# Optimization experiments

Measured on AMD Instinct MI355X. Metric: run time of the kernel, lower is better.

Reference implementation:

```python
import jax, jax.numpy as jnp
import numpy as np

N, E, F_IN, F_OUT = 20000, 8192, 128, 128


def setup_inputs() -> dict:
    key = jax.random.key(0)
    k1, k2, k3, k4, k5 = jax.random.split(key, 5)
    x = jax.random.normal(k1, (N, F_IN), dtype=jnp.float32)
    H = jax.random.uniform(k2, (N, E), dtype=jnp.float32)
    W = jax.random.uniform(k3, (E,), dtype=jnp.float32)  # diagonal of hyperedge weight matrix
    lin_w = jax.random.normal(k4, (F_OUT, F_IN), dtype=jnp.float32) * (1.0 / np.sqrt(F_IN))
    lin_b = jax.random.normal(k5, (F_OUT,), dtype=jnp.float32) * 0.01
    return {"x": x, "H": H, "W": W, "lin_w": lin_w, "lin_b": lin_b}


def reference(x, H, W, lin_w, lin_b):
    # Degrees
    Dv = jnp.clip(jnp.sum(H, axis=1), 1.0, None)          # [N] node degrees
    De = jnp.clip(jnp.sum(H, axis=0), 1.0, None)          # [E] hyperedge degrees
    dv_inv_sqrt = Dv ** -0.5                               # diag(Dv^-1/2)
    de_inv = 1.0 / De                                      # diag(De^-1)
    # Linear projection of node features
    xw = x @ lin_w.T + lin_b                               # [N, F_OUT]
    # L @ xw computed right-to-left: Dv^-1/2 H W De^-1 H^T Dv^-1/2 xw
    t = H.T @ (dv_inv_sqrt[:, None] * xw)                  # [E, F_OUT]
    t = (W * de_inv)[:, None] * t                          # diagonal W and De^-1 scaling
    out = dv_inv_sqrt[:, None] * (H @ t)                   # [N, F_OUT]
    return jax.nn.gelu(out, approximate=False)             # torch F.gelu default = exact erf
```

## Files before the change

### kernel.cpp

```cpp
#include <hip/hip_runtime.h>
#include <math.h>

static constexpr int N = 20000;
static constexpr int E = 8192;
static constexpr int F = 128;
static constexpr int NP = 20480;
static constexpr int NP2 = 20096;
static constexpr int PREP_BLOCKS = 1024;
static constexpr int PREP_REAL = 1000;
static constexpr int XW_BLOCKS = NP / 8;
static constexpr int SE_BLOCKS = 128;
static constexpr int KS_B = 8;
static constexpr int KS_C = 4;

typedef short bf16x8 __attribute__((ext_vector_type(8)));
typedef float f32x4 __attribute__((ext_vector_type(4)));

__device__ __forceinline__ float gelu_erf(float x) {
    return 0.5f * x * (1.0f + erff(x * 0.70710678118654752440f));
}
__device__ __forceinline__ ushort f2bf(float f) {
    unsigned u = __float_as_uint(f);
    return (ushort)((u + 0x7FFFu + ((u >> 16) & 1u)) >> 16);
}
__device__ __forceinline__ void gload16(const void* g, void* lds) {
    __builtin_amdgcn_global_load_lds(
        (const __attribute__((address_space(1))) unsigned int*)g,
        (__attribute__((address_space(3))) unsigned int*)lds, 16, 0, 0);
}

__global__ __launch_bounds__(256) void k_prep_xw(const float* __restrict__ H,
                                                 float* __restrict__ DeP,
                                                 ushort* __restrict__ Hbs,
                                                 const float* __restrict__ x,
                                                 const float* __restrict__ lin_w,
                                                 const float* __restrict__ lin_b,
                                                 ushort* __restrict__ yT) {
    __shared__ __align__(16) char smem[4096];
    const int tid = threadIdx.x;

    if (blockIdx.x < PREP_BLOCKS) {
        const int lane = tid & 63, wid = tid >> 6;
        const int r0 = blockIdx.x * 20;
        if (r0 >= N) {
            uint4 z = make_uint4(0, 0, 0, 0);
            for (int r = 0; r < 20; ++r) {
                ushort* orow = Hbs + (size_t)(r0 + r) * E;
#pragma unroll
                for (int j = 0; j < 4; ++j) *(uint4*)(orow + (j * 256 + tid) * 8) = z;
            }
            return;
        }
        float (*rp)[4] = (float(*)[4])smem;
        float4 ca[4][2];
#pragma unroll
        for (int j = 0; j < 4; ++j) {
            ca[j][0] = make_float4(0.f, 0.f, 0.f, 0.f);
            ca[j][1] = make_float4(0.f, 0.f, 0.f, 0.f);
        }
        for (int r = 0; r < 20; ++r) {
            const float* row = H + (size_t)(r0 + r) * E;
            float4 va[4], vb[4];
            float rs = 0.f;
#pragma unroll
            for (int j = 0; j < 4; ++j) {
                const float* base = row + (j * 256 + tid) * 8;
                va[j] = *(const float4*)(base);
                vb[j] = *(const float4*)(base + 4);
                ca[j][0].x += va[j].x; ca[j][0].y += va[j].y; ca[j][0].z += va[j].z; ca[j][0].w += va[j].w;
                ca[j][1].x += vb[j].x; ca[j][1].y += vb[j].y; ca[j][1].z += vb[j].z; ca[j][1].w += vb[j].w;
                rs += (va[j].x + va[j].y) + (va[j].z + va[j].w);
                rs += (vb[j].x + vb[j].y) + (vb[j].z + vb[j].w);
            }
#pragma unroll
            for (int off = 32; off > 0; off >>= 1) rs += __shfl_xor(rs, off, 64);
            if (lane == 0) rp[r][wid] = rs;
            __syncthreads();
            float scale = rsqrtf(fmaxf(rp[r][0] + rp[r][1] + rp[r][2] + rp[r][3], 1.f));
            ushort* orow = Hbs + (size_t)(r0 + r) * E;
#pragma unroll
            for (int j = 0; j < 4; ++j) {
                uint4 o;
                o.x = (unsigned)f2bf(va[j].x * scale) | ((unsigned)f2bf(va[j].y * scale) << 16);
                o.y = (unsigned)f2bf(va[j].z * scale) | ((unsigned)f2bf(va[j].w * scale) << 16);
                o.z = (unsigned)f2bf(vb[j].x * scale) | ((unsigned)f2bf(vb[j].y * scale) << 16);
                o.w = (unsigned)f2bf(vb[j].z * scale) | ((unsigned)f2bf(vb[j].w * scale) << 16);
                *(uint4*)(orow + (j * 256 + tid) * 8) = o;
            }
        }
        float* dp = DeP + (size_t)blockIdx.x * E;
#pragma unroll
        for (int j = 0; j < 4; ++j) {
            *(float4*)(dp + (j * 256 + tid) * 8) = ca[j][0];
            *(float4*)(dp + (j * 256 + tid) * 8 + 4) = ca[j][1];
        }
    } else {
        const int bxx = blockIdx.x - PREP_BLOCKS;
        const int r0 = bxx * 8;
        if (r0 >= N) {
            if (tid < 128) {
                uint4 z = make_uint4(0, 0, 0, 0);
                *(uint4*)(yT + (size_t)tid * NP + r0) = z;
            }
            return;
        }
        float* xs = (float*)smem;
#pragma unroll
        for (int c = 0; c < 4; ++c) {
            int lin = c * 256 + tid;
            xs[lin] = x[(size_t)r0 * F + lin];
        }
        __syncthreads();
        const int f = tid & 127, half = tid >> 7;
        float b = lin_b[f];
        float a0 = b, a1 = b, a2 = b, a3 = b;
        const float* xr = xs + (half * 4) * F;
        const float* lwr = lin_w + (size_t)f * F;
#pragma unroll 4
        for (int k = 0; k < F; k += 4) {
            float4 lw = *(const float4*)(lwr + k);
            a0 += xr[0 * F + k] * lw.x; a0 += xr[0 * F + k + 1] * lw.y;
            a0 += xr[0 * F + k + 2] * lw.z; a0 += xr[0 * F + k + 3] * lw.w;
            a1 += xr[1 * F + k] * lw.x; a1 += xr[1 * F + k + 1] * lw.y;
            a1 += xr[1 * F + k + 2] * lw.z; a1 += xr[1 * F + k + 3] * lw.w;
            a2 += xr[2 * F + k] * lw.x; a2 += xr[2 * F + k + 1] * lw.y;
            a2 += xr[2 * F + k + 2] * lw.z; a2 += xr[2 * F + k + 3] * lw.w;
            a3 += xr[3 * F + k] * lw.x; a3 += xr[3 * F + k + 1] * lw.y;
            a3 += xr[3 * F + k + 2] * lw.z; a3 += xr[3 * F + k + 3] * lw.w;
        }
        __syncthreads();
        ushort* tile = (ushort*)smem;
        tile[(half * 4 + 0) * F + f] = f2bf(a0);
        tile[(half * 4 + 1) * F + f] = f2bf(a1);
        tile[(half * 4 + 2) * F + f] = f2bf(a2);
        tile[(half * 4 + 3) * F + f] = f2bf(a3);
        __syncthreads();
        if (tid < 128) {
            unsigned u[4];
#pragma unroll
            for (int qq = 0; qq < 4; ++qq) {
                ushort lo = tile[(qq * 2 + 0) * F + tid];
                ushort hi = tile[(qq * 2 + 1) * F + tid];
                u[qq] = (unsigned)lo | ((unsigned)hi << 16);
            }
            uint4 o = make_uint4(u[0], u[1], u[2], u[3]);
            *(uint4*)(yT + (size_t)tid * NP + r0) = o;
        }
    }
}

__global__ void k_tst(const float* __restrict__ tB, const float* __restrict__ se,
                      ushort* __restrict__ tsT) {
    __shared__ __align__(16) char tl[8192];
    int tid = threadIdx.x;
    int r0 = (blockIdx.x >> 1) * 64;
    int c0 = (blockIdx.x & 1) * 64;
#pragma unroll
    for (int c = 0; c < 4; ++c) {
        int lin = c * 256 + tid;
        int row = lin >> 4, ch = lin & 15;
        size_t base = (size_t)(r0 + row) * F + c0 + ch * 4;
        float4 v = make_float4(0.f, 0.f, 0.f, 0.f);
#pragma unroll
        for (int ks = 0; ks < KS_B; ++ks) {
            float4 p = *(const float4*)(tB + (size_t)ks * E * F + base);
            v.x += p.x; v.y += p.y; v.z += p.z; v.w += p.w;
        }
        float s = se[r0 + row];
        ushort4 b;
        b.x = f2bf(v.x * s); b.y = f2bf(v.y * s); b.z = f2bf(v.z * s); b.w = f2bf(v.w * s);
        int key = ((row ^ (row >> 3)) & 7) << 4;
        *(ushort4*)(tl + row * 128 + ((ch * 8) ^ key)) = b;
    }
    __syncthreads();
#pragma unroll
    for (int c = 0; c < 2; ++c) {
        int lin = c * 256 + tid;
        int fl = lin >> 3, vch = lin & 7;
        unsigned u[4];
#pragma unroll
        for (int qq = 0; qq < 4; ++qq) {
            int r1 = vch * 8 + qq * 2, r2 = r1 + 1;
            ushort a = *(const ushort*)(tl + r1 * 128 + ((fl * 2) ^ (((r1 ^ (r1 >> 3)) & 7) << 4)));
            ushort b = *(const ushort*)(tl + r2 * 128 + ((fl * 2) ^ (((r2 ^ (r2 >> 3)) & 7) << 4)));
            u[qq] = (unsigned)a | ((unsigned)b << 16);
        }
        uint4 o = make_uint4(u[0], u[1], u[2], u[3]);
        *(uint4*)(tsT + (size_t)(c0 + fl) * E + r0 + vch * 8) = o;
    }
}

__global__ __launch_bounds__(256) void k_gemmB(const ushort* __restrict__ Hbs,
                                               const ushort* __restrict__ yT,
                                               float* __restrict__ tB,
                                               const float* __restrict__ DeP,
                                               const float* __restrict__ W,
                                               float* __restrict__ se) {
    __shared__ __align__(16) char lA[2][16384];
    __shared__ __align__(16) char lB[2][16384];
    const int tid = threadIdx.x;

    if (blockIdx.x < SE_BLOCKS) {
        float (*red)[64] = (float(*)[64])lA;
        const int c = blockIdx.x * 64 + (tid & 63);
        const int pg = tid >> 6;
        float s0 = 0.f, s1 = 0.f, s2 = 0.f, s3 = 0.f;
        int p = pg;
        for (; p + 12 < PREP_REAL; p += 16) {
            s0 += DeP[(size_t)(p +  0) * E + c];
            s1 += DeP[(size_t)(p +  4) * E + c];
            s2 += DeP[(size_t)(p +  8) * E + c];
            s3 += DeP[(size_t)(p + 12) * E + c];
        }
        for (; p < PREP_REAL; p += 4) s0 += DeP[(size_t)p * E + c];
        red[pg][tid & 63] = (s0 + s1) + (s2 + s3);
        __syncthreads();
        if (tid < 64) {
            float d = red[0][tid] + red[1][tid] + red[2][tid] + red[3][tid];
            int e = blockIdx.x * 64 + tid;
            se[e] = W[e] / fmaxf(d, 1.f);
        }
        return;
    }

    const int bx2 = blockIdx.x - SE_BLOCKS;
    const int sw = (bx2 & 7) * 64 + (bx2 >> 3);
    const int m0 = (sw & 63) * 128;
    const int ks = sw >> 6;
    const int k0 = ks * 2560;
    const int lane = tid & 63, w = tid >> 6;
    const int wm = (w & 1) * 64, wn = (w >> 1) * 64;
    const int lrow = lane & 15, g16 = (lane >> 4) * 16;
    const int NSTEP = 40;

    const int vq = tid >> 4;
    const int e8 = (tid & 15) * 8;
    const ushort* pa = Hbs + (size_t)(k0 + vq * 4) * E + m0 + e8;
    const int abase = e8 * 128 + ((vq * 8) ^ ((tid & 7) << 4));

    const int row8 = lane >> 3, ch8 = lane & 7;
    const ushort* gB = yT + (size_t)(w * 32 + row8) * NP + k0 + ((ch8 ^ row8) * 8);
    const int ldstB = w * 32 * 128;

    int aoff[4][2], boff[4][2];
#pragma unroll
    for (int f = 0; f < 4; ++f)
#pragma unroll
        for (int kk = 0; kk < 2; ++kk) {
            int ma = wm + f * 16 + lrow;
            aoff[f][kk] = ma * 128 + (((kk * 64) + g16) ^ (((ma >> 3) & 7) << 4));
            int nb = wn + f * 16 + lrow;
            boff[f][kk] = nb * 128 + (((kk * 64) + g16) ^ ((nb & 7) << 4));
        }

    f32x4 zero4 = {0.f, 0.f, 0.f, 0.f};
    f32x4 acc[4][4];
#pragma unroll
    for (int i = 0; i < 4; ++i)
#pragma unroll
        for (int j = 0; j < 4; ++j) acc[i][j] = zero4;

    uint4 ra[4];
#pragma unroll
    for (int r = 0; r < 4; ++r) ra[r] = *(const uint4*)(pa + (size_t)r * E);
    {
        const ushort* u0 = (const ushort*)&ra[0];
        const ushort* u1 = (const ushort*)&ra[1];
        const ushort* u2 = (const ushort*)&ra[2];
        const ushort* u3 = (const ushort*)&ra[3];
#pragma unroll
        for (int i = 0; i < 8; ++i) {
            uint2 wv;
            wv.x = (unsigned)u0[i] | ((unsigned)u1[i] << 16);
            wv.y = (unsigned)u2[i] | ((unsigned)u3[i] << 16);
            *(uint2*)(lA[0] + abase + i * 128) = wv;
        }
#pragma unroll
        for (int i = 0; i < 4; ++i)
            gload16(gB + (size_t)i * 8 * NP, lB[0] + ldstB + i * 1024);
    }
    pa += (size_t)64 * E;
#pragma unroll
    for (int r = 0; r < 4; ++r) ra[r] = *(const uint4*)(pa + (size_t)r * E);
    __syncthreads();

    for (int kt = 0; kt < NSTEP; ++kt) {
        const int cur = kt & 1;
        if (kt + 1 < NSTEP) {
            const ushort* u0 = (const ushort*)&ra[0];
            const ushort* u1 = (const ushort*)&ra[1];
            const ushort* u2 = (const ushort*)&ra[2];
            const ushort* u3 = (const ushort*)&ra[3];
#pragma unroll
            for (int i = 0; i < 8; ++i) {
                uint2 wv;
                wv.x = (unsigned)u0[i] | ((unsigned)u1[i] << 16);
                wv.y = (unsigned)u2[i] | ((unsigned)u3[i] << 16);
                *(uint2*)(lA[cur ^ 1] + abase + i * 128) = wv;
            }
            const int koff = (kt + 1) * 64;
#pragma unroll
            for (int i = 0; i < 4; ++i)
                gload16(gB + (size_t)i * 8 * NP + koff, lB[cur ^ 1] + ldstB + i * 1024);
        }
        if (kt + 2 < NSTEP) {
            pa += (size_t)64 * E;
#pragma unroll
            for (int r = 0; r < 4; ++r) ra[r] = *(const uint4*)(pa + (size_t)r * E);
        }
#pragma unroll
        for (int kk = 0; kk < 2; ++kk) {
            bf16x8 av[4], bv[4];
#pragma unroll
            for (int f = 0; f < 4; ++f) av[f] = *(const bf16x8*)(lA[cur] + aoff[f][kk]);
#pragma unroll
            for (int f = 0; f < 4; ++f) bv[f] = *(const bf16x8*)(lB[cur] + boff[f][kk]);
#pragma unroll
            for (int i = 0; i < 4; ++i)
#pragma unroll
                for (int j = 0; j < 4; ++j)
                    acc[i][j] = __builtin_amdgcn_mfma_f32_16x16x32_bf16(av[i], bv[j], acc[i][j], 0, 0, 0);
        }
        if (kt + 1 < NSTEP) __syncthreads();
    }
    float* plane = tB + (size_t)ks * E * F;
    const int orow = (lane >> 4) * 4, ocol = lane & 15;
#pragma unroll
    for (int i = 0; i < 4; ++i)
#pragma unroll
        for (int j = 0; j < 4; ++j) {
            int gm = m0 + wm + i * 16 + orow;
            int gn = wn + j * 16 + ocol;
#pragma unroll
            for (int q = 0; q < 4; ++q)
                plane[(size_t)(gm + q) * F + gn] = acc[i][j][q];
        }
}

__global__ __launch_bounds__(256) void k_gemmC(const ushort* __restrict__ Hbs,
                                               const ushort* __restrict__ tsT,
                                               float* __restrict__ C2P) {
    __shared__ __align__(16) char lA[2][16384];
    __shared__ __align__(16) char lB[2][16384];
    const int tid = threadIdx.x;
    const int qq_ = 78, rr_ = 4;
    const int xcd = blockIdx.x & 7, idx = blockIdx.x >> 3;
    const int sw = (xcd < rr_ ? xcd * (qq_ + 1) : rr_ * (qq_ + 1) + (xcd - rr_) * qq_) + idx;
    const int m0 = (sw % 157) * 128;
    const int ks = sw / 157;
    const int k0 = ks * 2048;
    const int lane = tid & 63, w = tid >> 6;
    const int wm = (w & 1) * 64, wn = (w >> 1) * 64;
    const int lrow = lane & 15, g16 = (lane >> 4) * 16;
    const int NSTEP = 32;

    const int row8 = lane >> 3, ch8 = lane & 7;
    const ushort* gA = Hbs + (size_t)(m0 + w * 32 + row8) * E + k0 + ((ch8 ^ row8) * 8);
    const ushort* gB = tsT + (size_t)(w * 32 + row8) * E + k0 + ((ch8 ^ row8) * 8);
    const int ldst = w * 32 * 128;

    int aoff[4][2], boff[4][2];
#pragma unroll
    for (int f = 0; f < 4; ++f)
#pragma unroll
        for (int kk = 0; kk < 2; ++kk) {
            int ma = wm + f * 16 + lrow;
            aoff[f][kk] = ma * 128 + (((kk * 64) + g16) ^ ((ma & 7) << 4));
            int nb = wn + f * 16 + lrow;
            boff[f][kk] = nb * 128 + (((kk * 64) + g16) ^ ((nb & 7) << 4));
        }

    f32x4 zero4 = {0.f, 0.f, 0.f, 0.f};
    f32x4 acc[4][4];
#pragma unroll
    for (int i = 0; i < 4; ++i)
#pragma unroll
        for (int j = 0; j < 4; ++j) acc[i][j] = zero4;

#pragma unroll
    for (int i = 0; i < 4; ++i) {
        gload16(gA + (size_t)i * 8 * E, lA[0] + ldst + i * 1024);
        gload16(gB + (size_t)i * 8 * E, lB[0] + ldst + i * 1024);
    }
    __syncthreads();

    for (int kt = 0; kt < NSTEP; ++kt) {
        const int cur = kt & 1;
        if (kt + 1 < NSTEP) {
            const int koff = (kt + 1) * 64;
#pragma unroll
            for (int i = 0; i < 4; ++i) {
                gload16(gA + (size_t)i * 8 * E + koff, lA[cur ^ 1] + ldst + i * 1024);
                gload16(gB + (size_t)i * 8 * E + koff, lB[cur ^ 1] + ldst + i * 1024);
            }
        }
#pragma unroll
        for (int kk = 0; kk < 2; ++kk) {
            bf16x8 av[4], bv[4];
#pragma unroll
            for (int f = 0; f < 4; ++f) av[f] = *(const bf16x8*)(lA[cur] + aoff[f][kk]);
#pragma unroll
            for (int f = 0; f < 4; ++f) bv[f] = *(const bf16x8*)(lB[cur] + boff[f][kk]);
#pragma unroll
            for (int i = 0; i < 4; ++i)
#pragma unroll
                for (int j = 0; j < 4; ++j)
                    acc[i][j] = __builtin_amdgcn_mfma_f32_16x16x32_bf16(av[i], bv[j], acc[i][j], 0, 0, 0);
        }
        if (kt + 1 < NSTEP) __syncthreads();
    }
    float* plane = C2P + (size_t)ks * NP2 * F;
    const int orow = (lane >> 4) * 4, ocol = lane & 15;
#pragma unroll
    for (int i = 0; i < 4; ++i)
#pragma unroll
        for (int j = 0; j < 4; ++j) {
            int gm = m0 + wm + i * 16 + orow;
            int gn = wn + j * 16 + ocol;
#pragma unroll
            for (int q = 0; q < 4; ++q)
                plane[(size_t)(gm + q) * F + gn] = acc[i][j][q];
        }
}

__global__ void k_fin_out(const float* __restrict__ C2P, float* __restrict__ out) {
    int i4 = blockIdx.x * 256 + threadIdx.x;
    if (i4 < N * F / 4) {
        float4 v = make_float4(0.f, 0.f, 0.f, 0.f);
#pragma unroll
        for (int ks = 0; ks < KS_C; ++ks) {
            float4 p = reinterpret_cast<const float4*>(C2P + (size_t)ks * NP2 * F)[i4];
            v.x += p.x; v.y += p.y; v.z += p.z; v.w += p.w;
        }
        float4 o;
        o.x = gelu_erf(v.x);
        o.y = gelu_erf(v.y);
        o.z = gelu_erf(v.z);
        o.w = gelu_erf(v.w);
        reinterpret_cast<float4*>(out)[i4] = o;
    }
}

extern "C" void kernel_launch(void* const* d_in, const int* in_sizes, int n_in,
                              void* d_out, int out_size, void* d_ws, size_t ws_size,
                              hipStream_t stream) {
    const float* x     = (const float*)d_in[0];
    const float* H     = (const float*)d_in[1];
    const float* W     = (const float*)d_in[2];
    const float* lin_w = (const float*)d_in[3];
    const float* lin_b = (const float*)d_in[4];
    float* out = (float*)d_out;

    char* ws = (char*)d_ws;
    ushort* Hbs = (ushort*)ws;
    ushort* yT  = (ushort*)(ws + 335544320);
    float*  tB  = (float*) (ws + 340787200);
    ushort* tsT = (ushort*)(ws + 374341632);
    float*  C2P = (float*) (ws + 376438784);
    float*  DeP = (float*) (ws + 417595392);
    float*  se  = (float*) (ws + 451149824);

    k_prep_xw<<<PREP_BLOCKS + XW_BLOCKS, 256, 0, stream>>>(H, DeP, Hbs, x, lin_w, lin_b, yT);
    k_gemmB<<<SE_BLOCKS + 64 * KS_B, 256, 0, stream>>>(Hbs, yT, tB, DeP, W, se);
    k_tst<<<(E / 64) * 2, 256, 0, stream>>>(tB, se, tsT);
    k_gemmC<<<157 * KS_C, 256, 0, stream>>>(Hbs, tsT, C2P);
    k_fin_out<<<(N * F / 4 + 255) / 256, 256, 0, stream>>>(C2P, out);
}
```

Baseline: 461.7 us.

## Store unscaled bf16 H and compute hyperedge degrees with MFMA in gemmB

H is now stored as raw bf16 without the per-row Dv^-1/2 scale. The Dv^-1/2 factor moves onto the projected features (new k_yscale kernel) and onto the final output before GELU. The per-block column partial sums and the separate SE reduction blocks are removed. Hyperedge degrees are instead accumulated inside gemmB with an extra MFMA against a ones vector, and the partials are summed in k_tst. This removes the 1000-row DeP partial buffer traffic and the in-prep syncs, in exchange for one extra small kernel, more MFMA work, and De computed from bf16-rounded H values.

```diff
diff --git a/kernel.cpp b/kernel.cpp
--- a/kernel.cpp
+++ b/kernel.cpp
@@ -6,10 +6,8 @@
 static constexpr int F = 128;
 static constexpr int NP = 20480;
 static constexpr int NP2 = 20096;
-static constexpr int PREP_BLOCKS = 1024;
-static constexpr int PREP_REAL = 1000;
+static constexpr int PREP_BLOCKS = 2048;
 static constexpr int XW_BLOCKS = NP / 8;
-static constexpr int SE_BLOCKS = 128;
 static constexpr int KS_B = 8;
 static constexpr int KS_C = 4;
 
@@ -19,9 +17,9 @@
 __device__ __forceinline__ float gelu_erf(float x) {
     return 0.5f * x * (1.0f + erff(x * 0.70710678118654752440f));
 }
-__device__ __forceinline__ ushort f2bf(float f) {
+__device__ __forceinline__ unsigned f2bf(float f) {
     unsigned u = __float_as_uint(f);
-    return (ushort)((u + 0x7FFFu + ((u >> 16) & 1u)) >> 16);
+    return (u + 0x7FFFu + ((u >> 16) & 1u)) >> 16;
 }
 __device__ __forceinline__ void gload16(const void* g, void* lds) {
     __builtin_amdgcn_global_load_lds(
@@ -30,7 +28,7 @@
 }
 
 __global__ __launch_bounds__(256) void k_prep_xw(const float* __restrict__ H,
-                                                 float* __restrict__ DeP,
+                                                 float* __restrict__ Dv,
                                                  ushort* __restrict__ Hbs,
                                                  const float* __restrict__ x,
                                                  const float* __restrict__ lin_w,
@@ -41,10 +39,10 @@
 
     if (blockIdx.x < PREP_BLOCKS) {
         const int lane = tid & 63, wid = tid >> 6;
-        const int r0 = blockIdx.x * 20;
+        const int r0 = blockIdx.x * 10;
         if (r0 >= N) {
             uint4 z = make_uint4(0, 0, 0, 0);
-            for (int r = 0; r < 20; ++r) {
+            for (int r = 0; r < 10; ++r) {
                 ushort* orow = Hbs + (size_t)(r0 + r) * E;
 #pragma unroll
                 for (int j = 0; j < 4; ++j) *(uint4*)(orow + (j * 256 + tid) * 8) = z;
@@ -52,48 +50,30 @@
             return;
         }
         float (*rp)[4] = (float(*)[4])smem;
-        float4 ca[4][2];
-#pragma unroll
-        for (int j = 0; j < 4; ++j) {
-            ca[j][0] = make_float4(0.f, 0.f, 0.f, 0.f);
-            ca[j][1] = make_float4(0.f, 0.f, 0.f, 0.f);
-        }
-        for (int r = 0; r < 20; ++r) {
+        for (int r = 0; r < 10; ++r) {
             const float* row = H + (size_t)(r0 + r) * E;
-            float4 va[4], vb[4];
+            ushort* orow = Hbs + (size_t)(r0 + r) * E;
             float rs = 0.f;
 #pragma unroll
             for (int j = 0; j < 4; ++j) {
                 const float* base = row + (j * 256 + tid) * 8;
-                va[j] = *(const float4*)(base);
-                vb[j] = *(const float4*)(base + 4);
-                ca[j][0].x += va[j].x; ca[j][0].y += va[j].y; ca[j][0].z += va[j].z; ca[j][0].w += va[j].w;
-                ca[j][1].x += vb[j].x; ca[j][1].y += vb[j].y; ca[j][1].z += vb[j].z; ca[j][1].w += vb[j].w;
-                rs += (va[j].x + va[j].y) + (va[j].z + va[j].w);
-                rs += (vb[j].x + vb[j].y) + (vb[j].z + vb[j].w);
+                float4 va = *(const float4*)(base);
+                float4 vb = *(const float4*)(base + 4);
+                rs += (va.x + va.y) + (va.z + va.w);
+                rs += (vb.x + vb.y) + (vb.z + vb.w);
+                uint4 o;
+                o.x = f2bf(va.x) | (f2bf(va.y) << 16);
+                o.y = f2bf(va.z) | (f2bf(va.w) << 16);
+                o.z = f2bf(vb.x) | (f2bf(vb.y) << 16);
+                o.w = f2bf(vb.z) | (f2bf(vb.w) << 16);
+                *(uint4*)(orow + (j * 256 + tid) * 8) = o;
             }
 #pragma unroll
             for (int off = 32; off > 0; off >>= 1) rs += __shfl_xor(rs, off, 64);
             if (lane == 0) rp[r][wid] = rs;
-            __syncthreads();
-            float scale = rsqrtf(fmaxf(rp[r][0] + rp[r][1] + rp[r][2] + rp[r][3], 1.f));
-            ushort* orow = Hbs + (size_t)(r0 + r) * E;
-#pragma unroll
-            for (int j = 0; j < 4; ++j) {
-                uint4 o;
-                o.x = (unsigned)f2bf(va[j].x * scale) | ((unsigned)f2bf(va[j].y * scale) << 16);
-                o.y = (unsigned)f2bf(va[j].z * scale) | ((unsigned)f2bf(va[j].w * scale) << 16);
-                o.z = (unsigned)f2bf(vb[j].x * scale) | ((unsigned)f2bf(vb[j].y * scale) << 16);
-                o.w = (unsigned)f2bf(vb[j].z * scale) | ((unsigned)f2bf(vb[j].w * scale) << 16);
-                *(uint4*)(orow + (j * 256 + tid) * 8) = o;
-            }
-        }
-        float* dp = DeP + (size_t)blockIdx.x * E;
-#pragma unroll
-        for (int j = 0; j < 4; ++j) {
-            *(float4*)(dp + (j * 256 + tid) * 8) = ca[j][0];
-            *(float4*)(dp + (j * 256 + tid) * 8 + 4) = ca[j][1];
-        }
+        }
+        __syncthreads();
+        if (tid < 10) Dv[r0 + tid] = rp[tid][0] + rp[tid][1] + rp[tid][2] + rp[tid][3];
     } else {
         const int bxx = blockIdx.x - PREP_BLOCKS;
         const int r0 = bxx * 8;
@@ -130,10 +110,10 @@
         }
         __syncthreads();
         ushort* tile = (ushort*)smem;
-        tile[(half * 4 + 0) * F + f] = f2bf(a0);
-        tile[(half * 4 + 1) * F + f] = f2bf(a1);
-        tile[(half * 4 + 2) * F + f] = f2bf(a2);
-        tile[(half * 4 + 3) * F + f] = f2bf(a3);
+        tile[(half * 4 + 0) * F + f] = (ushort)f2bf(a0);
+        tile[(half * 4 + 1) * F + f] = (ushort)f2bf(a1);
+        tile[(half * 4 + 2) * F + f] = (ushort)f2bf(a2);
+        tile[(half * 4 + 3) * F + f] = (ushort)f2bf(a3);
         __syncthreads();
         if (tid < 128) {
             unsigned u[4];
@@ -149,8 +129,37 @@
     }
 }
 
-__global__ void k_tst(const float* __restrict__ tB, const float* __restrict__ se,
-                      ushort* __restrict__ tsT) {
+__global__ void k_yscale(ushort* __restrict__ yT, const float* __restrict__ Dv) {
+    size_t g = (size_t)blockIdx.x * 256 + threadIdx.x;
+    size_t off = g * 8;
+    int v = (int)(off % NP);
+    uint4 u = *(uint4*)(yT + off);
+    float s[8];
+    if (v < N) {
+        float4 d0 = *(const float4*)(Dv + v);
+        float4 d1 = *(const float4*)(Dv + v + 4);
+        s[0] = rsqrtf(fmaxf(d0.x, 1.f)); s[1] = rsqrtf(fmaxf(d0.y, 1.f));
+        s[2] = rsqrtf(fmaxf(d0.z, 1.f)); s[3] = rsqrtf(fmaxf(d0.w, 1.f));
+        s[4] = rsqrtf(fmaxf(d1.x, 1.f)); s[5] = rsqrtf(fmaxf(d1.y, 1.f));
+        s[6] = rsqrtf(fmaxf(d1.z, 1.f)); s[7] = rsqrtf(fmaxf(d1.w, 1.f));
+    } else {
+#pragma unroll
+        for (int q = 0; q < 8; ++q) s[q] = 0.f;
+    }
+    unsigned wv[4] = {u.x, u.y, u.z, u.w};
+    uint4 o;
+    unsigned* ov = &o.x;
+#pragma unroll
+    for (int p = 0; p < 4; ++p) {
+        float lo = __uint_as_float(wv[p] << 16) * s[p * 2];
+        float hi = __uint_as_float(wv[p] & 0xFFFF0000u) * s[p * 2 + 1];
+        ov[p] = f2bf(lo) | (f2bf(hi) << 16);
+    }
+    *(uint4*)(yT + off) = o;
+}
+
+__global__ void k_tst(const float* __restrict__ tB, const float* __restrict__ DeP2,
+                      const float* __restrict__ W, ushort* __restrict__ tsT) {
     __shared__ __align__(16) char tl[8192];
     int tid = threadIdx.x;
     int r0 = (blockIdx.x >> 1) * 64;
@@ -166,9 +175,13 @@
             float4 p = *(const float4*)(tB + (size_t)ks * E * F + base);
             v.x += p.x; v.y += p.y; v.z += p.z; v.w += p.w;
         }
-        float s = se[r0 + row];
+        float d = 0.f;
+#pragma unroll
+        for (int ks = 0; ks < KS_B; ++ks) d += DeP2[(size_t)ks * E + r0 + row];
+        float s = W[r0 + row] / fmaxf(d, 1.f);
         ushort4 b;
-        b.x = f2bf(v.x * s); b.y = f2bf(v.y * s); b.z = f2bf(v.z * s); b.w = f2bf(v.w * s);
+        b.x = (ushort)f2bf(v.x * s); b.y = (ushort)f2bf(v.y * s);
+        b.z = (ushort)f2bf(v.z * s); b.w = (ushort)f2bf(v.w * s);
         int key = ((row ^ (row >> 3)) & 7) << 4;
         *(ushort4*)(tl + row * 128 + ((ch * 8) ^ key)) = b;
     }
@@ -193,38 +206,11 @@
 __global__ __launch_bounds__(256) void k_gemmB(const ushort* __restrict__ Hbs,
                                                const ushort* __restrict__ yT,
                                                float* __restrict__ tB,
-                                               const float* __restrict__ DeP,
-                                               const float* __restrict__ W,
-                                               float* __restrict__ se) {
+                                               float* __restrict__ DeP2) {
     __shared__ __align__(16) char lA[2][16384];
     __shared__ __align__(16) char lB[2][16384];
     const int tid = threadIdx.x;
-
-    if (blockIdx.x < SE_BLOCKS) {
-        float (*red)[64] = (float(*)[64])lA;
-        const int c = blockIdx.x * 64 + (tid & 63);
-        const int pg = tid >> 6;
-        float s0 = 0.f, s1 = 0.f, s2 = 0.f, s3 = 0.f;
-        int p = pg;
-        for (; p + 12 < PREP_REAL; p += 16) {
-            s0 += DeP[(size_t)(p +  0) * E + c];
-            s1 += DeP[(size_t)(p +  4) * E + c];
-            s2 += DeP[(size_t)(p +  8) * E + c];
-            s3 += DeP[(size_t)(p + 12) * E + c];
-        }
-        for (; p < PREP_REAL; p += 4) s0 += DeP[(size_t)p * E + c];
-        red[pg][tid & 63] = (s0 + s1) + (s2 + s3);
-        __syncthreads();
-        if (tid < 64) {
-            float d = red[0][tid] + red[1][tid] + red[2][tid] + red[3][tid];
-            int e = blockIdx.x * 64 + tid;
-            se[e] = W[e] / fmaxf(d, 1.f);
-        }
-        return;
-    }
-
-    const int bx2 = blockIdx.x - SE_BLOCKS;
-    const int sw = (bx2 & 7) * 64 + (bx2 >> 3);
+    const int sw = (blockIdx.x & 7) * 64 + (blockIdx.x >> 3);
     const int m0 = (sw & 63) * 128;
     const int ks = sw >> 6;
     const int k0 = ks * 2560;
@@ -255,10 +241,15 @@
 
     f32x4 zero4 = {0.f, 0.f, 0.f, 0.f};
     f32x4 acc[4][4];
-#pragma unroll
-    for (int i = 0; i < 4; ++i)
+    f32x4 deacc[4];
+    const short oneb = (short)0x3F80;
+    bf16x8 ones = {oneb, oneb, oneb, oneb, oneb, oneb, oneb, oneb};
+#pragma unroll
+    for (int i = 0; i < 4; ++i) {
+        deacc[i] = zero4;
 #pragma unroll
         for (int j = 0; j < 4; ++j) acc[i][j] = zero4;
+    }
 
     uint4 ra[4];
 #pragma unroll
@@ -317,6 +308,9 @@
             for (int f = 0; f < 4; ++f) bv[f] = *(const bf16x8*)(lB[cur] + boff[f][kk]);
 #pragma unroll
             for (int i = 0; i < 4; ++i)
+                deacc[i] = __builtin_amdgcn_mfma_f32_16x16x32_bf16(av[i], ones, deacc[i], 0, 0, 0);
+#pragma unroll
+            for (int i = 0; i < 4; ++i)
 #pragma unroll
                 for (int j = 0; j < 4; ++j)
                     acc[i][j] = __builtin_amdgcn_mfma_f32_16x16x32_bf16(av[i], bv[j], acc[i][j], 0, 0, 0);
@@ -335,6 +329,12 @@
             for (int q = 0; q < 4; ++q)
                 plane[(size_t)(gm + q) * F + gn] = acc[i][j][q];
         }
+    if (w < 2 && ocol == 0) {
+        float* dep = DeP2 + (size_t)ks * E + m0 + wm + orow;
+#pragma unroll
+        for (int i = 0; i < 4; ++i)
+            *(f32x4*)(dep + i * 16) = deacc[i];
+    }
 }
 
 __global__ __launch_bounds__(256) void k_gemmC(const ushort* __restrict__ Hbs,
@@ -423,9 +423,12 @@
         }
 }
 
-__global__ void k_fin_out(const float* __restrict__ C2P, float* __restrict__ out) {
+__global__ void k_fin_out(const float* __restrict__ C2P, const float* __restrict__ Dv,
+                          float* __restrict__ out) {
     int i4 = blockIdx.x * 256 + threadIdx.x;
     if (i4 < N * F / 4) {
+        int n = i4 >> 5;
+        float s = rsqrtf(fmaxf(Dv[n], 1.f));
         float4 v = make_float4(0.f, 0.f, 0.f, 0.f);
 #pragma unroll
         for (int ks = 0; ks < KS_C; ++ks) {
@@ -433,10 +436,10 @@
             v.x += p.x; v.y += p.y; v.z += p.z; v.w += p.w;
         }
         float4 o;
-        o.x = gelu_erf(v.x);
-        o.y = gelu_erf(v.y);
-        o.z = gelu_erf(v.z);
-        o.w = gelu_erf(v.w);
+        o.x = gelu_erf(s * v.x);
+        o.y = gelu_erf(s * v.y);
+        o.z = gelu_erf(s * v.z);
+        o.w = gelu_erf(s * v.w);
         reinterpret_cast<float4*>(out)[i4] = o;
     }
 }
@@ -452,17 +455,18 @@
     float* out = (float*)d_out;
 
     char* ws = (char*)d_ws;
-    ushort* Hbs = (ushort*)ws;
-    ushort* yT  = (ushort*)(ws + 335544320);
-    float*  tB  = (float*) (ws + 340787200);
-    ushort* tsT = (ushort*)(ws + 374341632);
-    float*  C2P = (float*) (ws + 376438784);
-    float*  DeP = (float*) (ws + 417595392);
-    float*  se  = (float*) (ws + 451149824);
-
-    k_prep_xw<<<PREP_BLOCKS + XW_BLOCKS, 256, 0, stream>>>(H, DeP, Hbs, x, lin_w, lin_b, yT);
-    k_gemmB<<<SE_BLOCKS + 64 * KS_B, 256, 0, stream>>>(Hbs, yT, tB, DeP, W, se);
-    k_tst<<<(E / 64) * 2, 256, 0, stream>>>(tB, se, tsT);
+    ushort* Hbs  = (ushort*)ws;
+    ushort* yT   = (ushort*)(ws + 335544320);
+    float*  tB   = (float*) (ws + 340787200);
+    ushort* tsT  = (ushort*)(ws + 374341632);
+    float*  C2P  = (float*) (ws + 376438784);
+    float*  DeP2 = (float*) (ws + 417595392);
+    float*  Dv   = (float*) (ws + 417857536);
+
+    k_prep_xw<<<PREP_BLOCKS + XW_BLOCKS, 256, 0, stream>>>(H, Dv, Hbs, x, lin_w, lin_b, yT);
+    k_yscale<<<(F * NP / 8) / 256, 256, 0, stream>>>(yT, Dv);
+    k_gemmB<<<64 * KS_B, 256, 0, stream>>>(Hbs, yT, tB, DeP2);
+    k_tst<<<(E / 64) * 2, 256, 0, stream>>>(tB, DeP2, W, tsT);
     k_gemmC<<<157 * KS_C, 256, 0, stream>>>(Hbs, tsT, C2P);
-    k_fin_out<<<(N * F / 4 + 255) / 256, 256, 0, stream>>>(C2P, out);
-}
+    k_fin_out<<<(N * F / 4 + 255) / 256, 256, 0, stream>>>(C2P, Dv, out);
+}
```

After: 445.8 us (median of 2 runs). 3.4% less time.
